# Kernel optimization log

Measured on AMD Instinct MI355X. Metric: run time of the kernel, lower is better.

Reference implementation:

```python
import jax, jax.numpy as jnp
import numpy as np


def setup_inputs() -> dict:
    key = jax.random.key(0)
    kq, kk, kv, ki, ks = jax.random.split(key, 5)
    B, H, S, D, VD, T = 2, 8, 2048, 64, 64, 128
    q = jax.random.normal(kq, (B, H, S, D), dtype=jnp.float32)
    k = jax.random.normal(kk, (B, H, S, D), dtype=jnp.float32)
    v = jax.random.normal(kv, (B, H, S, VD), dtype=jnp.float32)
    topk_indices = jax.random.randint(ki, (B, S, T), 0, S, dtype=jnp.int64)
    topk_scores = jax.random.uniform(ks, (B, S, T), dtype=jnp.float32)
    return {"q": q, "k": k, "v": v, "topk_indices": topk_indices,
            "topk_scores": topk_scores}


def reference(q, k, v, topk_indices, topk_scores):
    # q: (B,H,S,D), k: (B,H,S,D), v: (B,H,S,VD), topk_indices: (B,S,T)
    head_dim = q.shape[-1]
    scale = head_dim ** (-0.5)

    # Gather selected K/V per query directly (no O(S^2) expansion).
    # For each batch b: kb (H,S,D), idx (S,T) -> kb[:, idx, :] (H,S,T,D)
    gather = jax.vmap(lambda xb, ib: xb[:, ib, :])
    k_g = gather(k, topk_indices)  # (B,H,S,T,D)
    v_g = gather(v, topk_indices)  # (B,H,S,T,VD)

    # (B,H,S,T) scores
    attn_scores = jnp.einsum('bhsd,bhstd->bhst', q, k_g) * scale
    attn_weights = jax.nn.softmax(attn_scores, axis=-1)

    # reweight by indexer scores (broadcast over heads), then renormalize
    attn_weights = attn_weights * topk_scores[:, None, :, :]
    attn_weights = attn_weights / (attn_weights.sum(axis=-1, keepdims=True) + 1e-12)

    # (B,H,S,VD)
    output = jnp.einsum('bhst,bhstd->bhsd', attn_weights, v_g)
    return output
```

## Files before the change

### kernel.cpp

```cpp
#include <hip/hip_runtime.h>
#include <math.h>


#define BB 2
#define HH 8
#define SS 2048
#define DD 64
#define VDD 64
#define TT 128
#define SCALE 0.125f
#define NKV (BB * HH * SS * DD)

__device__ __forceinline__ float bf_lo(unsigned int u) {
    return __uint_as_float(u << 16);
}
__device__ __forceinline__ float bf_hi(unsigned int u) {
    return __uint_as_float(u);
}
__device__ __forceinline__ unsigned short f2bf_rne(float f) {
    unsigned int u = __float_as_uint(f);
    u += 0x7FFFu + ((u >> 16) & 1u);
    return (unsigned short)(u >> 16);
}

__global__ __launch_bounds__(256) void cvt_kv_bf16(
    const float* __restrict__ k, const float* __restrict__ v,
    unsigned int* __restrict__ kb, unsigned int* __restrict__ vb)
{
    int i = (blockIdx.x * 256 + threadIdx.x) * 4;
    if (i >= NKV) return;
    float4 kf = *(const float4*)(k + i);
    float4 vf = *(const float4*)(v + i);
    unsigned int k0 = (unsigned int)f2bf_rne(kf.x) | ((unsigned int)f2bf_rne(kf.y) << 16);
    unsigned int k1 = (unsigned int)f2bf_rne(kf.z) | ((unsigned int)f2bf_rne(kf.w) << 16);
    unsigned int v0 = (unsigned int)f2bf_rne(vf.x) | ((unsigned int)f2bf_rne(vf.y) << 16);
    unsigned int v1 = (unsigned int)f2bf_rne(vf.z) | ((unsigned int)f2bf_rne(vf.w) << 16);
    *(uint2*)(kb + i / 2) = make_uint2(k0, k1);
    *(uint2*)(vb + i / 2) = make_uint2(v0, v1);
}

__global__ __launch_bounds__(256, 4) void dsa_sparse_attn_bf16(
    const float* __restrict__ q,
    const unsigned int* __restrict__ kb,
    const unsigned int* __restrict__ vb,
    const int* __restrict__ topk_idx,
    const float* __restrict__ topk_sc,
    float* __restrict__ out)
{
    const int tid  = threadIdx.x;
    const int wave = tid >> 6;
    const int lane = tid & 63;
    const int h    = lane & 7;
    const int g    = lane >> 3;

    const int plane = blockIdx.x & 15;
    const int s     = (blockIdx.x >> 4) * 4 + wave;
    const int b     = plane >> 3;

    const float*        qp  = q  + ((size_t)plane * SS + s) * DD;
    const unsigned int* kp  = kb + (size_t)plane * SS * (DD / 2);
    const unsigned int* vp  = vb + (size_t)plane * SS * (VDD / 2);
    const int*          ip  = topk_idx + ((size_t)b * SS + s) * TT;
    const float*        scp = topk_sc  + ((size_t)b * SS + s) * TT;
    float*              op  = out + ((size_t)plane * SS + s) * VDD;

    __shared__ uint2 s_wi[4][TT];

    float sc0 = scp[lane];
    float sc1 = scp[64 + lane];
    s_wi[wave][lane].y      = (unsigned int)ip[lane];
    s_wi[wave][64 + lane].y = (unsigned int)ip[64 + lane];

    float4 qa = *(const float4*)(qp + h * 8);
    float4 qb = *(const float4*)(qp + h * 8 + 4);

    __syncthreads();

    #pragma unroll
    for (int tc = 0; tc < 16; ++tc) {
        int t   = tc * 8 + g;
        int idx = (int)s_wi[wave][t].y;
        uint4 kk = *(const uint4*)(kp + (size_t)idx * 32 + h * 4);
        float acc;
        acc  = qa.x * bf_lo(kk.x) + qa.y * bf_hi(kk.x);
        acc += qa.z * bf_lo(kk.y) + qa.w * bf_hi(kk.y);
        acc += qb.x * bf_lo(kk.z) + qb.y * bf_hi(kk.z);
        acc += qb.z * bf_lo(kk.w) + qb.w * bf_hi(kk.w);
        acc += __shfl_xor(acc, 1);
        acc += __shfl_xor(acc, 2);
        acc += __shfl_xor(acc, 4);
        if (h == 0) s_wi[wave][t].x = __float_as_uint(acc * SCALE);
    }
    __syncthreads();

    float a0 = __uint_as_float(s_wi[wave][lane].x);
    float a1 = __uint_as_float(s_wi[wave][64 + lane].x);
    float m = fmaxf(a0, a1);
    #pragma unroll
    for (int off = 32; off >= 1; off >>= 1)
        m = fmaxf(m, __shfl_xor(m, off));
    float e0 = __expf(a0 - m) * sc0;
    float e1 = __expf(a1 - m) * sc1;
    float sum = e0 + e1;
    #pragma unroll
    for (int off = 32; off >= 1; off >>= 1)
        sum += __shfl_xor(sum, off);
    float inv = 1.0f / (sum + 1e-12f);
    s_wi[wave][lane].x      = __float_as_uint(e0 * inv);
    s_wi[wave][64 + lane].x = __float_as_uint(e1 * inv);
    __syncthreads();

    float a[8] = {0.f, 0.f, 0.f, 0.f, 0.f, 0.f, 0.f, 0.f};
    #pragma unroll
    for (int i = 0; i < 16; ++i) {
        uint2 wi = s_wi[wave][i * 8 + g];
        float w  = __uint_as_float(wi.x);
        int  idx = (int)wi.y;
        uint4 u = *(const uint4*)(vp + (size_t)idx * 32 + h * 4);
        a[0] = fmaf(w, bf_lo(u.x), a[0]);  a[1] = fmaf(w, bf_hi(u.x), a[1]);
        a[2] = fmaf(w, bf_lo(u.y), a[2]);  a[3] = fmaf(w, bf_hi(u.y), a[3]);
        a[4] = fmaf(w, bf_lo(u.z), a[4]);  a[5] = fmaf(w, bf_hi(u.z), a[5]);
        a[6] = fmaf(w, bf_lo(u.w), a[6]);  a[7] = fmaf(w, bf_hi(u.w), a[7]);
    }
    #pragma unroll
    for (int j = 0; j < 8; ++j) {
        a[j] += __shfl_xor(a[j], 8);
        a[j] += __shfl_xor(a[j], 16);
        a[j] += __shfl_xor(a[j], 32);
    }
    if (g == 0) {
        *(float4*)(op + h * 8)     = make_float4(a[0], a[1], a[2], a[3]);
        *(float4*)(op + h * 8 + 4) = make_float4(a[4], a[5], a[6], a[7]);
    }
}

__global__ __launch_bounds__(256, 4) void dsa_sparse_attn_f32(
    const float* __restrict__ q,
    const float* __restrict__ k,
    const float* __restrict__ v,
    const int* __restrict__ topk_idx,
    const float* __restrict__ topk_sc,
    float* __restrict__ out)
{
    const int tid  = threadIdx.x;
    const int wave = tid >> 6;
    const int lane = tid & 63;
    const int plane = blockIdx.x & 15;
    const int s     = (blockIdx.x >> 4) * 4 + wave;
    const int b     = plane >> 3;

    const float* qp  = q + ((size_t)plane * SS + s) * DD;
    const float* kp  = k + (size_t)plane * SS * DD;
    const float* vp  = v + (size_t)plane * SS * VDD;
    const int*   ip  = topk_idx + ((size_t)b * SS + s) * TT;
    const float* scp = topk_sc  + ((size_t)b * SS + s) * TT;
    float*       op  = out + ((size_t)plane * SS + s) * VDD;

    __shared__ int   s_idx[4][TT];
    __shared__ float s_w[4][TT];

    float sc0 = scp[lane];
    float sc1 = scp[64 + lane];
    s_idx[wave][lane]      = ip[lane];
    s_idx[wave][64 + lane] = ip[64 + lane];

    const int l = lane & 3;
    const int g = lane >> 2;
    float4 qf[4];
    #pragma unroll
    for (int j = 0; j < 4; ++j) qf[j] = *(const float4*)(qp + l * 4 + 16 * j);
    __syncthreads();

    #pragma unroll
    for (int tc = 0; tc < 8; ++tc) {
        int t = tc * 16 + g;
        const float* krow = kp + (size_t)s_idx[wave][t] * DD;
        float acc = 0.f;
        #pragma unroll
        for (int j = 0; j < 4; ++j) {
            float4 kf = *(const float4*)(krow + l * 4 + 16 * j);
            acc += qf[j].x * kf.x + qf[j].y * kf.y + qf[j].z * kf.z + qf[j].w * kf.w;
        }
        acc += __shfl_xor(acc, 1);
        acc += __shfl_xor(acc, 2);
        if (l == 0) s_w[wave][t] = acc * SCALE;
    }
    __syncthreads();

    float a0 = s_w[wave][lane];
    float a1 = s_w[wave][64 + lane];
    float m = fmaxf(a0, a1);
    #pragma unroll
    for (int off = 32; off >= 1; off >>= 1) m = fmaxf(m, __shfl_xor(m, off));
    float e0 = __expf(a0 - m) * sc0;
    float e1 = __expf(a1 - m) * sc1;
    float sum = e0 + e1;
    #pragma unroll
    for (int off = 32; off >= 1; off >>= 1) sum += __shfl_xor(sum, off);
    float inv = 1.0f / (sum + 1e-12f);
    s_w[wave][lane]      = e0 * inv;
    s_w[wave][64 + lane] = e1 * inv;
    __syncthreads();

    float acc = 0.f;
    #pragma unroll 8
    for (int t = 0; t < TT; ++t)
        acc = fmaf(s_w[wave][t], vp[(size_t)s_idx[wave][t] * VDD + lane], acc);
    op[lane] = acc;
}

extern "C" void kernel_launch(void* const* d_in, const int* in_sizes, int n_in,
                              void* d_out, int out_size, void* d_ws, size_t ws_size,
                              hipStream_t stream) {
    const float* q   = (const float*)d_in[0];
    const float* k   = (const float*)d_in[1];
    const float* v   = (const float*)d_in[2];
    const int*   idx = (const int*)d_in[3];
    const float* sc  = (const float*)d_in[4];
    float*       out = (float*)d_out;

    const size_t need = (size_t)NKV * 2 * 2;
    if (ws_size >= need) {
        unsigned int* kb = (unsigned int*)d_ws;
        unsigned int* vb = kb + NKV / 2;
        hipLaunchKernelGGL(cvt_kv_bf16, dim3(NKV / 4 / 256), dim3(256), 0, stream,
                           k, v, kb, vb);
        hipLaunchKernelGGL(dsa_sparse_attn_bf16, dim3(8192), dim3(256), 0, stream,
                           q, kb, vb, idx, sc, out);
    } else {
        hipLaunchKernelGGL(dsa_sparse_attn_f32, dim3(8192), dim3(256), 0, stream,
                           q, k, v, idx, sc, out);
    }
}
```

Measured before the change: 130.7 us.

## Keep indices, scores and weights in registers; remove LDS and block barriers

The bf16 attention kernel no longer stages top-k indices and softmax weights through shared memory with three __syncthreads. Indices and indexer scores are broadcast to each lane with wave shuffles, and QK scores stay in per-lane register arrays. Softmax max and sum are reduced in registers and then across lane groups. This removes block-wide barriers and LDS traffic, so each wave runs independently, at the cost of higher register pressure (around 48 extra registers) and some additional shuffles.

```diff
diff --git a/kernel.cpp b/kernel.cpp
--- a/kernel.cpp
+++ b/kernel.cpp
@@ -64,23 +64,26 @@
     const float*        scp = topk_sc  + ((size_t)b * SS + s) * TT;
     float*              op  = out + ((size_t)plane * SS + s) * VDD;
 
-    __shared__ uint2 s_wi[4][TT];
-
-    float sc0 = scp[lane];
-    float sc1 = scp[64 + lane];
-    s_wi[wave][lane].y      = (unsigned int)ip[lane];
-    s_wi[wave][64 + lane].y = (unsigned int)ip[64 + lane];
-
+    int   iv0 = ip[lane];
+    int   iv1 = ip[64 + lane];
+    float sv0 = scp[lane];
+    float sv1 = scp[64 + lane];
     float4 qa = *(const float4*)(qp + h * 8);
     float4 qb = *(const float4*)(qp + h * 8 + 4);
 
-    __syncthreads();
-
-    #pragma unroll
-    for (int tc = 0; tc < 16; ++tc) {
-        int t   = tc * 8 + g;
-        int idx = (int)s_wi[wave][t].y;
-        uint4 kk = *(const uint4*)(kp + (size_t)idx * 32 + h * 4);
+    int   idxr[16];
+    float scr[16];
+    #pragma unroll
+    for (int tc = 0; tc < 16; ++tc) {
+        int t = tc * 8 + g;
+        if (tc < 8) { idxr[tc] = __shfl(iv0, t);      scr[tc] = __shfl(sv0, t); }
+        else        { idxr[tc] = __shfl(iv1, t - 64); scr[tc] = __shfl(sv1, t - 64); }
+    }
+
+    float sco[16];
+    #pragma unroll
+    for (int tc = 0; tc < 16; ++tc) {
+        uint4 kk = *(const uint4*)(kp + (size_t)idxr[tc] * 32 + h * 4);
         float acc;
         acc  = qa.x * bf_lo(kk.x) + qa.y * bf_hi(kk.x);
         acc += qa.z * bf_lo(kk.y) + qa.w * bf_hi(kk.y);
@@ -89,34 +92,32 @@
         acc += __shfl_xor(acc, 1);
         acc += __shfl_xor(acc, 2);
         acc += __shfl_xor(acc, 4);
-        if (h == 0) s_wi[wave][t].x = __float_as_uint(acc * SCALE);
-    }
-    __syncthreads();
-
-    float a0 = __uint_as_float(s_wi[wave][lane].x);
-    float a1 = __uint_as_float(s_wi[wave][64 + lane].x);
-    float m = fmaxf(a0, a1);
-    #pragma unroll
-    for (int off = 32; off >= 1; off >>= 1)
-        m = fmaxf(m, __shfl_xor(m, off));
-    float e0 = __expf(a0 - m) * sc0;
-    float e1 = __expf(a1 - m) * sc1;
-    float sum = e0 + e1;
-    #pragma unroll
-    for (int off = 32; off >= 1; off >>= 1)
-        sum += __shfl_xor(sum, off);
+        sco[tc] = acc * SCALE;
+    }
+
+    float m = sco[0];
+    #pragma unroll
+    for (int tc = 1; tc < 16; ++tc) m = fmaxf(m, sco[tc]);
+    m = fmaxf(m, __shfl_xor(m, 8));
+    m = fmaxf(m, __shfl_xor(m, 16));
+    m = fmaxf(m, __shfl_xor(m, 32));
+    float sum = 0.f;
+    #pragma unroll
+    for (int tc = 0; tc < 16; ++tc) {
+        float e = __expf(sco[tc] - m) * scr[tc];
+        sco[tc] = e;
+        sum += e;
+    }
+    sum += __shfl_xor(sum, 8);
+    sum += __shfl_xor(sum, 16);
+    sum += __shfl_xor(sum, 32);
     float inv = 1.0f / (sum + 1e-12f);
-    s_wi[wave][lane].x      = __float_as_uint(e0 * inv);
-    s_wi[wave][64 + lane].x = __float_as_uint(e1 * inv);
-    __syncthreads();
 
     float a[8] = {0.f, 0.f, 0.f, 0.f, 0.f, 0.f, 0.f, 0.f};
     #pragma unroll
-    for (int i = 0; i < 16; ++i) {
-        uint2 wi = s_wi[wave][i * 8 + g];
-        float w  = __uint_as_float(wi.x);
-        int  idx = (int)wi.y;
-        uint4 u = *(const uint4*)(vp + (size_t)idx * 32 + h * 4);
+    for (int tc = 0; tc < 16; ++tc) {
+        float w = sco[tc] * inv;
+        uint4 u = *(const uint4*)(vp + (size_t)idxr[tc] * 32 + h * 4);
         a[0] = fmaf(w, bf_lo(u.x), a[0]);  a[1] = fmaf(w, bf_hi(u.x), a[1]);
         a[2] = fmaf(w, bf_lo(u.y), a[2]);  a[3] = fmaf(w, bf_hi(u.y), a[3]);
         a[4] = fmaf(w, bf_lo(u.z), a[4]);  a[5] = fmaf(w, bf_hi(u.z), a[5]);
```

Result: no change. 132.7 us (+1.5%).
